# Kernel optimization log

Hardware: AMD Instinct MI355X
Metric: run time of the kernel (lower is better)

Reference implementation:

```python
import math
import jax, jax.numpy as jnp
import numpy as np

B, N, D, H, PREFIX = 2, 2048, 2048, 16, 512
HD = D // H
ROPE_BASE = 10000.0

def _rope(x):
    # x: [b, h, n, d]; rotate-half RoPE with positions 0..n-1
    d = x.shape[-1]
    n = x.shape[-2]
    inv_freq = 1.0 / (ROPE_BASE ** (jnp.arange(0, d, 2, dtype=jnp.float32) / d))  # [d/2]
    pos = jnp.arange(n, dtype=jnp.float32)
    freqs = pos[:, None] * inv_freq[None, :]            # [n, d/2]
    cos, sin = jnp.cos(freqs), jnp.sin(freqs)
    x1, x2 = x[..., : d // 2], x[..., d // 2 :]
    return jnp.concatenate([x1 * cos - x2 * sin, x2 * cos + x1 * sin], axis=-1).astype(x.dtype)

def setup_inputs() -> dict:
    key = jax.random.key(0)
    ks = jax.random.split(key, 6)
    x = jax.random.normal(ks[0], (B, N, D), dtype=jnp.float32)
    prefix_k = jax.random.normal(ks[1], (B, H, PREFIX, HD), dtype=jnp.float32)
    prefix_v = jax.random.normal(ks[2], (B, H, PREFIX, HD), dtype=jnp.float32)
    Wqkv = jax.random.normal(ks[3], (D, 3 * D), dtype=jnp.float32) * (D ** -0.5)
    bqkv = jnp.zeros((3 * D,), dtype=jnp.float32)
    Wff = jax.random.normal(ks[4], (D, D), dtype=jnp.float32) * (D ** -0.5)
    bff = jnp.zeros((D,), dtype=jnp.float32)
    # causal mask over current tokens; prefix (cache) columns fully visible
    causal = jnp.tril(jnp.ones((N, N), dtype=jnp.int32))
    mask = jnp.concatenate([jnp.ones((N, PREFIX), dtype=jnp.int32), causal], axis=1)[None, None]  # [1,1,N,N+PREFIX]
    return {"x": x, "mask": mask, "prefix_k": prefix_k, "prefix_v": prefix_v,
            "Wqkv": Wqkv, "bqkv": bqkv, "Wff": Wff, "bff": bff}

def reference(x, mask, prefix_k, prefix_v, Wqkv, bqkv, Wff, bff):
    b, n, d = x.shape
    h = prefix_k.shape[1]
    hd = d // h
    qkv = (x @ Wqkv + bqkv).reshape(b, n, 3, h, hd)      # 'b n (c h d)'
    qkv = jnp.transpose(qkv, (2, 0, 3, 1, 4))            # -> c b h n d
    q, k, v = qkv[0], qkv[1], qkv[2]
    k = jnp.concatenate([prefix_k, k], axis=2)           # [b,h,kt,hd]
    v = jnp.concatenate([prefix_v, v], axis=2)
    next_prefix_kv = jnp.stack([k, v])                   # cached BEFORE rope (as in source)
    q = _rope(q)
    k = _rope(k)
    scores = jnp.einsum('bhqd,bhkd->bhqk', q, k) / math.sqrt(hd)
    scores = jnp.where(mask == 0, jnp.finfo(scores.dtype).min, scores)
    probs = jax.nn.softmax(scores, axis=-1)              # dropout_prob=0.0 -> identity
    attn_o = jnp.einsum('bhqk,bhkd->bhqd', probs, v)
    attn_o = jnp.transpose(attn_o, (0, 2, 1, 3)).reshape(b, n, d)
    return attn_o @ Wff + bff, next_prefix_kv
```

## Files before the change

kernel.cpp:

```cpp
#include <hip/hip_runtime.h>
#include <hip/hip_bf16.h>
#include <stdint.h>

#define TPB 256

using f32x4 = __attribute__((ext_vector_type(4))) float;
using s16x8 = __attribute__((ext_vector_type(8))) short;
using s16x4 = __attribute__((ext_vector_type(4))) short;

__device__ __forceinline__ short f2bf(float f){
  union { float f; uint32_t u; } v; v.f = f;
  uint32_t u = v.u;
  uint32_t r = (u + 0x7fffu + ((u >> 16) & 1u)) >> 16;
  return (short)(uint16_t)r;
}
__device__ __forceinline__ float bf2f(short b){
  union { uint32_t u; float f; } v; v.u = ((uint32_t)(uint16_t)b) << 16;
  return v.f;
}
__device__ __forceinline__ f32x4 mfma16(s16x8 a, s16x8 b, f32x4 c){
  return __builtin_amdgcn_mfma_f32_16x16x32_bf16(a, b, c, 0, 0, 0);
}

#define AS1(p) ((const __attribute__((address_space(1))) void*)(p))
#define AS3(p) ((__attribute__((address_space(3))) void*)(p))

__global__ void k_cvt_bf16(const float* __restrict__ src, short* __restrict__ dst, int n8){
  int i = blockIdx.x * TPB + threadIdx.x;
  if (i >= n8) return;
  const float4* s4 = (const float4*)src;
  float4 a = s4[2*i], b = s4[2*i+1];
  s16x8 o;
  o[0]=f2bf(a.x); o[1]=f2bf(a.y); o[2]=f2bf(a.z); o[3]=f2bf(a.w);
  o[4]=f2bf(b.x); o[5]=f2bf(b.y); o[6]=f2bf(b.z); o[7]=f2bf(b.w);
  *(s16x8*)(dst + 8*(size_t)i) = o;
}

__global__ void k_trans_cvt(const float* __restrict__ W, short* __restrict__ WT, int K, int Nn){
  __shared__ float ls[32][33];
  int k0 = blockIdx.x * 32, n0 = blockIdx.y * 32;
  int c = threadIdx.x & 31, i = threadIdx.x >> 5;
#pragma unroll
  for (int rr = 0; rr < 4; rr++){
    int row = i*4 + rr;
    ls[row][c] = W[(size_t)(k0+row)*Nn + n0 + c];
  }
  __syncthreads();
#pragma unroll
  for (int rr = 0; rr < 4; rr++){
    int ro = i*4 + rr;
    WT[(size_t)(n0+ro)*K + k0 + c] = f2bf(ls[c][ro]);
  }
}

__global__ void __launch_bounds__(512, 2) k_gemm16(
    const short* __restrict__ A, const short* __restrict__ Bt,
    const float* __restrict__ bias,
    float* __restrict__ kvout,
    short* __restrict__ qpre, short* __restrict__ kpre, short* __restrict__ vpre)
{
  __shared__ __align__(16) short As[3][8192];
  __shared__ __align__(16) short Bs[3][8192];
  const int tid = threadIdx.x;
  const int w = tid >> 6, l = tid & 63;
  const int lrow = l & 15, lg = l >> 4;
  const int wm = w >> 2, wn = w & 3;
  const int lid = blockIdx.x + (int)gridDim.x * blockIdx.y;
  const int swz = (lid & 7) * 48 + (lid >> 3);
  const int m0 = (swz & 15) << 8, n0 = (swz >> 4) << 8;
  constexpr int NT = 64;

  f32x4 acc[8][4] = {};

  size_t offA0, offA1, offB0, offB1;
  {
    const int s0 = tid, s1 = 512 + tid;
    const int gr0 = ((s0 >> 6) << 4) + (s0 & 15), c80 = ((s0 >> 4) & 3) * 8;
    const int gr1 = ((s1 >> 6) << 4) + (s1 & 15), c81 = ((s1 >> 4) & 3) * 8;
    offA0 = (size_t)(m0 + gr0) * 2048 + c80;
    offA1 = (size_t)(m0 + gr1) * 2048 + c81;
    offB0 = (size_t)(n0 + gr0) * 2048 + c80;
    offB1 = (size_t)(n0 + gr1) * 2048 + c81;
  }
  const int dst0 = w * 1024;
  const int dst1 = 8192 + w * 1024;

#define STG_A0(sl, t_) __builtin_amdgcn_global_load_lds(AS1(A  + offA0 + (size_t)(t_)*32), AS3((char*)As[sl] + dst0), 16, 0, 0)
#define STG_A1(sl, t_) __builtin_amdgcn_global_load_lds(AS1(A  + offA1 + (size_t)(t_)*32), AS3((char*)As[sl] + dst1), 16, 0, 0)
#define STG_B0(sl, t_) __builtin_amdgcn_global_load_lds(AS1(Bt + offB0 + (size_t)(t_)*32), AS3((char*)Bs[sl] + dst0), 16, 0, 0)
#define STG_B1(sl, t_) __builtin_amdgcn_global_load_lds(AS1(Bt + offB1 + (size_t)(t_)*32), AS3((char*)Bs[sl] + dst1), 16, 0, 0)

  STG_A0(0,0); STG_A1(0,0); STG_B0(0,0); STG_B1(0,0);
  STG_A0(1,1); STG_A1(1,1); STG_B0(1,1); STG_B1(1,1);

  const int rdo  = lg * 256 + lrow * 16;
  const int aoff = wm * 8192 + rdo;
  const int boff = wn * 4096 + rdo;

  int slot = 0;
  for (int t = 0; t < NT; ++t){
    if (t < NT-1) asm volatile("s_waitcnt vmcnt(4)" ::: "memory");
    else          asm volatile("s_waitcnt vmcnt(0)" ::: "memory");
    __builtin_amdgcn_s_barrier();
    asm volatile("" ::: "memory");
    const int sslot = (slot == 0) ? 2 : slot - 1;
    const bool st = (t+2) < NT;
    const char* ab = (const char*)As[slot];
    const char* bb = (const char*)Bs[slot];

    s16x8 bfr[4];
#pragma unroll
    for (int ni = 0; ni < 4; ni++)
      bfr[ni] = *(const s16x8*)(bb + boff + ni*1024);
    s16x8 af[4];
#pragma unroll
    for (int mi = 0; mi < 4; mi++)
      af[mi] = *(const s16x8*)(ab + aoff + mi*1024);
    if (st){ STG_A0(sslot, t+2); STG_B0(sslot, t+2); }
    __builtin_amdgcn_s_setprio(1);
#pragma unroll
    for (int mi = 0; mi < 4; mi++)
#pragma unroll
      for (int ni = 0; ni < 4; ni++)
        acc[mi][ni] = mfma16(af[mi], bfr[ni], acc[mi][ni]);
    __builtin_amdgcn_s_setprio(0);
    asm volatile("" ::: "memory");
    __builtin_amdgcn_s_barrier();
    asm volatile("" ::: "memory");

    s16x8 af2[4];
#pragma unroll
    for (int mi = 0; mi < 4; mi++)
      af2[mi] = *(const s16x8*)(ab + aoff + (mi+4)*1024);
    if (st){ STG_A1(sslot, t+2); STG_B1(sslot, t+2); }
    __builtin_amdgcn_s_setprio(1);
#pragma unroll
    for (int mi = 0; mi < 4; mi++)
#pragma unroll
      for (int ni = 0; ni < 4; ni++)
        acc[mi+4][ni] = mfma16(af2[mi], bfr[ni], acc[mi+4][ni]);
    __builtin_amdgcn_s_setprio(0);
    slot = (slot == 2) ? 0 : slot + 1;
  }
#undef STG_A0
#undef STG_A1
#undef STG_B0
#undef STG_B1

#pragma unroll
  for (int mi = 0; mi < 8; mi++){
#pragma unroll
    for (int ni = 0; ni < 4; ni++){
      const int c  = n0 + wn*64 + ni*16 + lrow;
      const int mb = m0 + wm*128 + mi*16 + lg*4;
      const float bv = bias[c];
      const int s = c >> 11, h = (c >> 7) & 15, tt = c & 127;
#pragma unroll
      for (int r = 0; r < 4; r++){
        const int m = mb + r;
        const int b = m >> 11, n = m & 2047;
        const int bh = b*16 + h;
        const float val = acc[mi][ni][r] + bv;
        if (s == 0){
          qpre[((size_t)bh*2048 + n)*128 + tt] = f2bf(val);
        } else if (s == 1){
          kvout[((size_t)bh*2560 + 512 + n)*128 + tt] = val;
          kpre[((size_t)bh*2048 + n)*128 + tt] = f2bf(val);
        } else {
          kvout[(size_t)(32 + bh)*327680 + (size_t)(512 + n)*128 + tt] = val;
          vpre[((size_t)bh*2048 + n)*128 + tt] = f2bf(val);
        }
      }
    }
  }
}

template<int EPI>
__global__ void __launch_bounds__(512, 2) k_gemm8(
    const short* __restrict__ A, const short* __restrict__ Bt,
    int Nn, int K,
    const float* __restrict__ bias,
    float* __restrict__ outp,
    float* __restrict__ kvout,
    short* __restrict__ qpre, short* __restrict__ kpre, short* __restrict__ vpre)
{
  __shared__ __align__(16) short As[3][16384];
  __shared__ __align__(16) short Bs[3][8192];
  const int tid = threadIdx.x;
  const int w = tid >> 6, l = tid & 63;
  const int lrow = l & 15, lg = l >> 4;
  const int wm = w >> 1, wn = w & 1;
  const int m0 = blockIdx.x << 8, n0 = blockIdx.y << 7;
  const int NT = K >> 6;

  f32x4 acc[4][4] = {};

#define STAGE_A(slot, t, j) do {                                             \
    int chunk = ((w*4 + (j)) << 6) + l;                                      \
    int row = chunk >> 3, cc = chunk & 7;                                    \
    __builtin_amdgcn_global_load_lds(                                        \
      AS1(A + (size_t)(m0+row)*K + (t)*64 + ((cc ^ (row&7)) << 3)),          \
      AS3(&As[slot][(w*4 + (j)) << 9]), 16, 0, 0);                           \
  } while(0)
#define STAGE_B(slot, t, j) do {                                             \
    int chunk = ((w*2 + (j)) << 6) + l;                                      \
    int row = chunk >> 3, cc = chunk & 7;                                    \
    __builtin_amdgcn_global_load_lds(                                        \
      AS1(Bt + (size_t)(n0+row)*K + (t)*64 + ((cc ^ (row&7)) << 3)),         \
      AS3(&Bs[slot][(w*2 + (j)) << 9]), 16, 0, 0);                           \
  } while(0)

  STAGE_A(0,0,0); STAGE_A(0,0,1); STAGE_A(0,0,2); STAGE_A(0,0,3);
  STAGE_B(0,0,0); STAGE_B(0,0,1);
  STAGE_A(1,1,0); STAGE_A(1,1,1); STAGE_A(1,1,2); STAGE_A(1,1,3);
  STAGE_B(1,1,0); STAGE_B(1,1,1);

  int slot = 0;
  for (int t = 0; t < NT; ++t){
    if (t < NT-1) asm volatile("s_waitcnt vmcnt(6)" ::: "memory");
    else          asm volatile("s_waitcnt vmcnt(0)" ::: "memory");
    __builtin_amdgcn_s_barrier();
    asm volatile("" ::: "memory");
    const int sslot = (slot == 0) ? 2 : slot - 1;
    const bool st = (t+2) < NT;
    const char* ab = (const char*)As[slot];
    const char* bb = (const char*)Bs[slot];

    s16x8 bfr[4][2];
#pragma unroll
    for (int ni = 0; ni < 4; ni++){
      int row = wn*64 + ni*16 + lrow;
#pragma unroll
      for (int ks = 0; ks < 2; ks++)
        bfr[ni][ks] = *(const s16x8*)(bb + row*128 + ((ks*64 + lg*16) ^ ((row&7)<<4)));
    }
    s16x8 af[2][2];
#pragma unroll
    for (int mi = 0; mi < 2; mi++){
      int row = wm*64 + mi*16 + lrow;
#pragma unroll
      for (int ks = 0; ks < 2; ks++)
        af[mi][ks] = *(const s16x8*)(ab + row*128 + ((ks*64 + lg*16) ^ ((row&7)<<4)));
    }
    if (st){ STAGE_A(sslot,t+2,0); STAGE_A(sslot,t+2,1); STAGE_B(sslot,t+2,0); }
    __builtin_amdgcn_s_setprio(1);
#pragma unroll
    for (int ks = 0; ks < 2; ks++)
#pragma unroll
      for (int mi = 0; mi < 2; mi++)
#pragma unroll
        for (int ni = 0; ni < 4; ni++)
          acc[mi][ni] = mfma16(af[mi][ks], bfr[ni][ks], acc[mi][ni]);
    __builtin_amdgcn_s_setprio(0);
    asm volatile("" ::: "memory");
    __builtin_amdgcn_s_barrier();
    asm volatile("" ::: "memory");

    s16x8 af2[2][2];
#pragma unroll
    for (int mi = 0; mi < 2; mi++){
      int row = wm*64 + (mi+2)*16 + lrow;
#pragma unroll
      for (int ks = 0; ks < 2; ks++)
        af2[mi][ks] = *(const s16x8*)(ab + row*128 + ((ks*64 + lg*16) ^ ((row&7)<<4)));
    }
    if (st){ STAGE_A(sslot,t+2,2); STAGE_A(sslot,t+2,3); STAGE_B(sslot,t+2,1); }
    __builtin_amdgcn_s_setprio(1);
#pragma unroll
    for (int ks = 0; ks < 2; ks++)
#pragma unroll
      for (int mi = 0; mi < 2; mi++)
#pragma unroll
        for (int ni = 0; ni < 4; ni++)
          acc[mi+2][ni] = mfma16(af2[mi][ks], bfr[ni][ks], acc[mi+2][ni]);
    __builtin_amdgcn_s_setprio(0);
    slot = (slot == 2) ? 0 : slot + 1;
  }
#undef STAGE_A
#undef STAGE_B

#pragma unroll
  for (int mi = 0; mi < 4; mi++){
#pragma unroll
    for (int ni = 0; ni < 4; ni++){
      const int c  = n0 + wn*64 + ni*16 + lrow;
      const int mb = m0 + wm*64 + mi*16 + lg*4;
      const float bv = bias[c];
      if (EPI == 1){
#pragma unroll
        for (int r = 0; r < 4; r++)
          outp[(size_t)(mb+r)*Nn + c] = acc[mi][ni][r] + bv;
      } else {
        const int s = c >> 11, h = (c >> 7) & 15, tt = c & 127;
#pragma unroll
        for (int r = 0; r < 4; r++){
          const int m = mb + r;
          const int b = m >> 11, n = m & 2047;
          const int bh = b*16 + h;
          const float val = acc[mi][ni][r] + bv;
          if (s == 0){
            qpre[((size_t)bh*2048 + n)*128 + tt] = f2bf(val);
          } else if (s == 1){
            kvout[((size_t)bh*2560 + 512 + n)*128 + tt] = val;
            kpre[((size_t)bh*2048 + n)*128 + tt] = f2bf(val);
          } else {
            kvout[(size_t)(32 + bh)*327680 + (size_t)(512 + n)*128 + tt] = val;
            vpre[((size_t)bh*2048 + n)*128 + tt] = f2bf(val);
          }
        }
      }
    }
  }
}

__global__ void k_rope_q(const short* __restrict__ src, short* __restrict__ dst){
  int gid = blockIdx.x * TPB + threadIdx.x;
  int j = gid & 63; size_t row = gid >> 6;
  int n = (int)(row & 2047);
  float x1 = bf2f(src[row*128 + j]);
  float x2 = bf2f(src[row*128 + 64 + j]);
  float invf = __expf((float)j * (-9.210340371976184f/64.0f));
  float sn, cs; __sincosf((float)n * invf, &sn, &cs);
  const float sc = 0.088388347648318447f;
  dst[row*128 + j]      = f2bf((x1*cs - x2*sn) * sc);
  dst[row*128 + 64 + j] = f2bf((x2*cs + x1*sn) * sc);
}

__global__ void k_rope_k_new(const short* __restrict__ kpre, short* __restrict__ kr){
  int gid = blockIdx.x * TPB + threadIdx.x;
  int j = gid & 63; size_t row = gid >> 6;
  int bh = (int)(row >> 11), n = (int)(row & 2047);
  int pos = 512 + n;
  float x1 = bf2f(kpre[row*128 + j]);
  float x2 = bf2f(kpre[row*128 + 64 + j]);
  float invf = __expf((float)j * (-9.210340371976184f/64.0f));
  float sn, cs; __sincosf((float)pos * invf, &sn, &cs);
  size_t drow = (size_t)bh*2560 + pos;
  kr[drow*128 + j]      = f2bf(x1*cs - x2*sn);
  kr[drow*128 + 64 + j] = f2bf(x2*cs + x1*sn);
}

__global__ void k_rope_k_prefix(const float* __restrict__ pk, float* __restrict__ kvout0,
                                short* __restrict__ kr){
  int gid = blockIdx.x * TPB + threadIdx.x;
  int j = gid & 63; size_t row = gid >> 6;
  int bh = (int)(row >> 9), p = (int)(row & 511);
  float x1 = pk[row*128 + j];
  float x2 = pk[row*128 + 64 + j];
  size_t orow = (size_t)bh*2560 + p;
  kvout0[orow*128 + j]      = x1;
  kvout0[orow*128 + 64 + j] = x2;
  float invf = __expf((float)j * (-9.210340371976184f/64.0f));
  float sn, cs; __sincosf((float)p * invf, &sn, &cs);
  kr[orow*128 + j]      = f2bf(x1*cs - x2*sn);
  kr[orow*128 + 64 + j] = f2bf(x2*cs + x1*sn);
}

__global__ void k_v_prefix(const float* __restrict__ pv, float* __restrict__ kvout1,
                           short* __restrict__ vT){
  __shared__ float ls[32][129];
  int bh = blockIdx.x >> 4, pt = blockIdx.x & 15;
  int p0 = pt*32, tid = threadIdx.x;
#pragma unroll
  for (int i = 0; i < 16; i++){
    int idx = i*TPB + tid; int p = idx >> 7, t = idx & 127;
    float v = pv[((size_t)bh*512 + p0 + p)*128 + t];
    ls[p][t] = v;
    kvout1[((size_t)bh*2560 + p0 + p)*128 + t] = v;
  }
  __syncthreads();
#pragma unroll
  for (int i = 0; i < 16; i++){
    int idx = i*TPB + tid; int t = idx >> 5, p = idx & 31;
    vT[((size_t)bh*128 + t)*2560 + p0 + p] = f2bf(ls[p][t]);
  }
}

__global__ void k_v_new(const short* __restrict__ vpre, short* __restrict__ vT){
  __shared__ float ls[32][129];
  int bh = blockIdx.x >> 6, nt = blockIdx.x & 63;
  int n0 = nt*32, tid = threadIdx.x;
#pragma unroll
  for (int i = 0; i < 16; i++){
    int idx = i*TPB + tid; int p = idx >> 7, t = idx & 127;
    ls[p][t] = bf2f(vpre[((size_t)bh*2048 + n0 + p)*128 + t]);
  }
  __syncthreads();
#pragma unroll
  for (int i = 0; i < 16; i++){
    int idx = i*TPB + tid; int t = idx >> 5, p = idx & 31;
    vT[((size_t)bh*128 + t)*2560 + 512 + n0 + p] = f2bf(ls[p][t]);
  }
}

__global__ void __launch_bounds__(256, 2) k_attn(
    const short* __restrict__ qr, const short* __restrict__ kr,
    const short* __restrict__ vT, short* __restrict__ attno)
{
  __shared__ short Ks[2][64*128];
  __shared__ short VTs[2][128*64];
  __shared__ short Ps[4][16*64];
  const int bh = blockIdx.x;
  const int pA = blockIdx.y, pB = 31 - pA;
  const int nA = 9 + pA, nTot = 49;
  const int tid = threadIdx.x, w = tid >> 6, l = tid & 63;
  const int lrow = l & 15, lg = l >> 4;
  const int b = bh >> 4, h = bh & 15;

  s16x8 qfA[4], qfB[4];
  {
    const size_t rA = (size_t)bh*2048 + pA*64 + w*16 + lrow;
    const size_t rB = (size_t)bh*2048 + pB*64 + w*16 + lrow;
#pragma unroll
    for (int ks = 0; ks < 4; ks++){
      qfA[ks] = *(const s16x8*)&qr[rA*128 + ks*32 + lg*8];
      qfB[ks] = *(const s16x8*)&qr[rB*128 + ks*32 + lg*8];
    }
  }

#define STAGE_KV(buf, kv0s) do {                                                    \
    _Pragma("unroll")                                                               \
    for (int i_ = 0; i_ < 4; i_++){                                                 \
      int chunk = i_*256 + tid;                                                     \
      int row = chunk >> 4, cc = (chunk & 15) ^ (row & 7);                          \
      __builtin_amdgcn_global_load_lds(                                             \
        AS1(kr + ((size_t)bh*2560 + (kv0s) + row)*128 + cc*8),                      \
        AS3((char*)Ks[buf] + (i_*256 + w*64)*16), 16, 0, 0);                        \
    }                                                                               \
    _Pragma("unroll")                                                               \
    for (int i_ = 0; i_ < 4; i_++){                                                 \
      int chunk = i_*256 + tid;                                                     \
      int row = chunk >> 3, cc = (chunk & 7) ^ (row & 7);                           \
      __builtin_amdgcn_global_load_lds(                                             \
        AS1(vT + ((size_t)bh*128 + row)*2560 + (kv0s) + cc*8),                      \
        AS3((char*)VTs[buf] + (i_*256 + w*64)*16), 16, 0, 0);                       \
    }                                                                               \
  } while(0)

  STAGE_KV(0, 0);
  STAGE_KV(1, 64);

  char* psw = (char*)&Ps[w][0];
  int g = 0;
#pragma unroll 2
  for (int ph = 0; ph < 2; ph++){
    const int qt = ph ? pB : pA;
    const int n = 9 + qt;
    const int qbw = qt*64 + w*16;
    f32x4 acc[8] = {};
    float mr = -1e30f, lsum = 0.f;

    for (int t = 0; t < n; t++, g++){
      if (g+1 < nTot) asm volatile("s_waitcnt vmcnt(8)" ::: "memory");
      else            asm volatile("s_waitcnt vmcnt(0)" ::: "memory");
      __builtin_amdgcn_s_barrier();
      asm volatile("" ::: "memory");
      const char* kb_ = (const char*)Ks[g&1];
      const char* vb_ = (const char*)VTs[g&1];
      const int kv0 = t*64;

      f32x4 sf[4];
      __builtin_amdgcn_s_setprio(1);
#pragma unroll
      for (int kb = 0; kb < 4; kb++){
        f32x4 s = {0.f,0.f,0.f,0.f};
#pragma unroll
        for (int ks = 0; ks < 4; ks++){
          int row  = kb*16 + lrow;
          int colb = ks*64 + lg*16;
          s16x8 kf = *(const s16x8*)(kb_ + row*256 + (colb ^ ((row&7)<<4)));
          s = mfma16(kf, ph ? qfB[ks] : qfA[ks], s);
        }
        sf[kb] = s;
      }
      __builtin_amdgcn_s_setprio(0);

      const int qme = 512 + qbw + lrow;
      if (kv0 + 63 > 512 + qbw){
#pragma unroll
        for (int kb = 0; kb < 4; kb++)
#pragma unroll
          for (int r = 0; r < 4; r++){
            int kg = kv0 + kb*16 + lg*4 + r;
            if (kg > qme) sf[kb][r] = -1e30f;
          }
      }

      float m_ = fmaxf(
          fmaxf(fmaxf(fmaxf(sf[0][0],sf[0][1]),fmaxf(sf[0][2],sf[0][3])),
                fmaxf(fmaxf(sf[1][0],sf[1][1]),fmaxf(sf[1][2],sf[1][3]))),
          fmaxf(fmaxf(fmaxf(sf[2][0],sf[2][1]),fmaxf(sf[2][2],sf[2][3])),
                fmaxf(fmaxf(sf[3][0],sf[3][1]),fmaxf(sf[3][2],sf[3][3]))));
      m_ = fmaxf(m_, __shfl_xor(m_, 16));
      m_ = fmaxf(m_, __shfl_xor(m_, 32));

      if (__any(m_ > mr + 8.f)){
        float mnew = fmaxf(mr, m_);
        float sc = __expf(mr - mnew);
        mr = mnew;
        lsum *= sc;
        float scr[4];
#pragma unroll
        for (int r = 0; r < 4; r++)
          scr[r] = __shfl(sc, (l & 48) | (lg*4 + r));
#pragma unroll
        for (int dt = 0; dt < 8; dt++)
#pragma unroll
          for (int r = 0; r < 4; r++) acc[dt][r] *= scr[r];
      }

#pragma unroll
      for (int kb = 0; kb < 4; kb++){
        float p0 = __expf(sf[kb][0] - mr);
        float p1 = __expf(sf[kb][1] - mr);
        float p2 = __expf(sf[kb][2] - mr);
        float p3 = __expf(sf[kb][3] - mr);
        lsum += (p0+p1)+(p2+p3);
        s16x4 pk4 = { f2bf(p0), f2bf(p1), f2bf(p2), f2bf(p3) };
        *(s16x4*)(psw + (lrow*128 + ((kb*32 + lg*8) ^ ((lrow&7)<<4)))) = pk4;
      }

      __builtin_amdgcn_s_setprio(1);
#pragma unroll
      for (int kp = 0; kp < 2; kp++){
        s16x8 pa = *(const s16x8*)(psw + (lrow*128 + ((kp*64 + lg*16) ^ ((lrow&7)<<4))));
#pragma unroll
        for (int dt = 0; dt < 8; dt++){
          int vrow = dt*16 + lrow;
          int vcolb = kp*64 + lg*16;
          s16x8 vf = *(const s16x8*)(vb_ + vrow*128 + (vcolb ^ ((vrow&7)<<4)));
          acc[dt] = mfma16(pa, vf, acc[dt]);
        }
      }
      __builtin_amdgcn_s_setprio(0);

      asm volatile("" ::: "memory");
      __builtin_amdgcn_s_barrier();
      asm volatile("" ::: "memory");
      const int gg = g + 2;
      if (gg < nTot){
        const int kvs = (gg < nA ? gg : gg - nA) * 64;
        STAGE_KV(g&1, kvs);
      }
    }

    float ls_ = lsum;
    ls_ += __shfl_xor(ls_, 16);
    ls_ += __shfl_xor(ls_, 32);
    float linv[4];
#pragma unroll
    for (int r = 0; r < 4; r++)
      linv[r] = 1.f / __shfl(ls_, (l & 48) | (lg*4 + r));
#pragma unroll
    for (int dt = 0; dt < 8; dt++){
#pragma unroll
      for (int r = 0; r < 4; r++){
        int nrow = qbw + lg*4 + r;
        int dcol = h*128 + dt*16 + lrow;
        attno[((size_t)b*2048 + nrow)*2048 + dcol] = f2bf(acc[dt][r] * linv[r]);
      }
    }
  }
#undef STAGE_KV
}

extern "C" void kernel_launch(void* const* d_in, const int* in_sizes, int n_in,
                              void* d_out, int out_size, void* d_ws, size_t ws_size,
                              hipStream_t stream)
{
  const float* x    = (const float*)d_in[0];
  const float* pk   = (const float*)d_in[2];
  const float* pv   = (const float*)d_in[3];
  const float* Wqkv = (const float*)d_in[4];
  const float* bqkv = (const float*)d_in[5];
  const float* Wff  = (const float*)d_in[6];
  const float* bff  = (const float*)d_in[7];
  float* out   = (float*)d_out;
  float* kvout = out + 8388608;

  char* ws = (char*)d_ws;
  short* xb    = (short*)(ws);
  short* wqkvT = (short*)(ws + 16777216);
  short* wffT  = (short*)(ws + 41943040);
  short* qpre  = (short*)(ws + 50331648);
  short* kpre  = (short*)(ws + 67108864);
  short* vpre  = (short*)(ws + 83886080);
  short* qrp   = (short*)(ws + 100663296);
  short* krp   = (short*)(ws + 117440512);
  short* vTp   = (short*)(ws + 138412032);
  short* attno = (short*)(ws + 159383552);

  k_cvt_bf16<<<4096, TPB, 0, stream>>>(x, xb, 1048576);
  k_trans_cvt<<<dim3(64, 192), TPB, 0, stream>>>(Wqkv, wqkvT, 2048, 6144);
  k_trans_cvt<<<dim3(64, 64),  TPB, 0, stream>>>(Wff,  wffT,  2048, 2048);

  k_gemm16<<<dim3(16, 24), 512, 0, stream>>>(xb, wqkvT, bqkv, kvout, qpre, kpre, vpre);

  k_rope_q<<<16384, TPB, 0, stream>>>(qpre, qrp);
  k_rope_k_new<<<16384, TPB, 0, stream>>>(kpre, krp);
  k_rope_k_prefix<<<4096, TPB, 0, stream>>>(pk, kvout, krp);
  k_v_prefix<<<512, TPB, 0, stream>>>(pv, kvout + (size_t)32*327680, vTp);
  k_v_new<<<2048, TPB, 0, stream>>>(vpre, vTp);

  k_attn<<<dim3(32, 16), TPB, 0, stream>>>(qrp, krp, vTp, attno);

  k_gemm8<1><<<dim3(16, 16), 512, 0, stream>>>(attno, wffT, 2048, 2048, bff,
                                               out, nullptr, nullptr, nullptr, nullptr);
}
```

Measured before the change: 351.1 us.

## Restructure QKV GEMM mainloop to double-buffered K=64 tiles with quarter-step staging

Replaces the three-slot K=32 pipeline in the QKV projection GEMM with a two-buffer scheme that stages K=64 per iteration. Each iteration is split into four sub-phases that interleave LDS fragment reads, async global-to-LDS loads for the next tile, and MFMA blocks. This halves the outer loop count and aims to overlap prefetch more evenly with compute. In exchange it adds more barriers per iteration, and the prefetch distance drops to one tile.

```diff
diff --git a/kernel.cpp b/kernel.cpp
--- a/kernel.cpp
+++ b/kernel.cpp
@@ -59,8 +59,8 @@
     float* __restrict__ kvout,
     short* __restrict__ qpre, short* __restrict__ kpre, short* __restrict__ vpre)
 {
-  __shared__ __align__(16) short As[3][8192];
-  __shared__ __align__(16) short Bs[3][8192];
+  __shared__ __align__(16) short As[2][16384];
+  __shared__ __align__(16) short Bs[2][16384];
   const int tid = threadIdx.x;
   const int w = tid >> 6, l = tid & 63;
   const int lrow = l & 15, lg = l >> 4;
@@ -68,55 +68,49 @@
   const int lid = blockIdx.x + (int)gridDim.x * blockIdx.y;
   const int swz = (lid & 7) * 48 + (lid >> 3);
   const int m0 = (swz & 15) << 8, n0 = (swz >> 4) << 8;
-  constexpr int NT = 64;
+  constexpr int NT = 32;
 
   f32x4 acc[8][4] = {};
 
-  size_t offA0, offA1, offB0, offB1;
-  {
-    const int s0 = tid, s1 = 512 + tid;
-    const int gr0 = ((s0 >> 6) << 4) + (s0 & 15), c80 = ((s0 >> 4) & 3) * 8;
-    const int gr1 = ((s1 >> 6) << 4) + (s1 & 15), c81 = ((s1 >> 4) & 3) * 8;
-    offA0 = (size_t)(m0 + gr0) * 2048 + c80;
-    offA1 = (size_t)(m0 + gr1) * 2048 + c81;
-    offB0 = (size_t)(n0 + gr0) * 2048 + c80;
-    offB1 = (size_t)(n0 + gr1) * 2048 + c81;
-  }
-  const int dst0 = w * 1024;
-  const int dst1 = 8192 + w * 1024;
-
-#define STG_A0(sl, t_) __builtin_amdgcn_global_load_lds(AS1(A  + offA0 + (size_t)(t_)*32), AS3((char*)As[sl] + dst0), 16, 0, 0)
-#define STG_A1(sl, t_) __builtin_amdgcn_global_load_lds(AS1(A  + offA1 + (size_t)(t_)*32), AS3((char*)As[sl] + dst1), 16, 0, 0)
-#define STG_B0(sl, t_) __builtin_amdgcn_global_load_lds(AS1(Bt + offB0 + (size_t)(t_)*32), AS3((char*)Bs[sl] + dst0), 16, 0, 0)
-#define STG_B1(sl, t_) __builtin_amdgcn_global_load_lds(AS1(Bt + offB1 + (size_t)(t_)*32), AS3((char*)Bs[sl] + dst1), 16, 0, 0)
-
-  STG_A0(0,0); STG_A1(0,0); STG_B0(0,0); STG_B1(0,0);
-  STG_A0(1,1); STG_A1(1,1); STG_B0(1,1); STG_B1(1,1);
-
-  const int rdo  = lg * 256 + lrow * 16;
-  const int aoff = wm * 8192 + rdo;
-  const int boff = wn * 4096 + rdo;
-
-  int slot = 0;
+  const size_t gA0 = (size_t)(m0 + w*16 + (l & 15)) * 2048 + (l >> 4) * 8;
+  const size_t gB0 = (size_t)(n0 + w*16 + (l & 15)) * 2048 + (l >> 4) * 8;
+
+#define STG_A(buf, t_, j_, kk_)                                              \
+  __builtin_amdgcn_global_load_lds(                                          \
+    AS1(A + gA0 + (size_t)(j_)*262144 + (size_t)(t_)*64 + (kk_)*32),         \
+    AS3(&As[buf][((j_)*8 + w)*1024 + (kk_)*512]), 16, 0, 0)
+#define STG_B(buf, t_, j_, kk_)                                              \
+  __builtin_amdgcn_global_load_lds(                                          \
+    AS1(Bt + gB0 + (size_t)(j_)*262144 + (size_t)(t_)*64 + (kk_)*32),        \
+    AS3(&Bs[buf][((j_)*8 + w)*1024 + (kk_)*512]), 16, 0, 0)
+
+  STG_A(0, 0, 0, 0); STG_A(0, 0, 1, 0);
+  STG_B(0, 0, 0, 0); STG_B(0, 0, 1, 0);
+  STG_A(0, 0, 0, 1); STG_A(0, 0, 1, 1);
+  STG_B(0, 0, 0, 1); STG_B(0, 0, 1, 1);
+  asm volatile("s_waitcnt vmcnt(4)" ::: "memory");
+  __builtin_amdgcn_s_barrier();
+  asm volatile("" ::: "memory");
+
+  const int rdo = lg * 256 + lrow * 16;
+
+  int cb = 0;
   for (int t = 0; t < NT; ++t){
-    if (t < NT-1) asm volatile("s_waitcnt vmcnt(4)" ::: "memory");
-    else          asm volatile("s_waitcnt vmcnt(0)" ::: "memory");
-    __builtin_amdgcn_s_barrier();
-    asm volatile("" ::: "memory");
-    const int sslot = (slot == 0) ? 2 : slot - 1;
-    const bool st = (t+2) < NT;
-    const char* ab = (const char*)As[slot];
-    const char* bb = (const char*)Bs[slot];
-
-    s16x8 bfr[4];
+    const int nb = cb ^ 1;
+    const bool st = (t + 1) < NT;
+    const char* ab = (const char*)As[cb];
+    const char* bb = (const char*)Bs[cb];
+    s16x8 bfr[4], af[4];
+
 #pragma unroll
     for (int ni = 0; ni < 4; ni++)
-      bfr[ni] = *(const s16x8*)(bb + boff + ni*1024);
-    s16x8 af[4];
-#pragma unroll
-    for (int mi = 0; mi < 4; mi++)
-      af[mi] = *(const s16x8*)(ab + aoff + mi*1024);
-    if (st){ STG_A0(sslot, t+2); STG_B0(sslot, t+2); }
+      bfr[ni] = *(const s16x8*)(bb + (wn*4 + ni)*2048 + rdo);
+#pragma unroll
+    for (int mi = 0; mi < 4; mi++)
+      af[mi] = *(const s16x8*)(ab + (wm*8 + mi)*2048 + rdo);
+    if (st){ STG_A(nb, t+1, 0, 0); STG_A(nb, t+1, 1, 0); }
+    __builtin_amdgcn_s_barrier();
+    asm volatile("" ::: "memory");
     __builtin_amdgcn_s_setprio(1);
 #pragma unroll
     for (int mi = 0; mi < 4; mi++)
@@ -128,24 +122,67 @@
     __builtin_amdgcn_s_barrier();
     asm volatile("" ::: "memory");
 
-    s16x8 af2[4];
-#pragma unroll
-    for (int mi = 0; mi < 4; mi++)
-      af2[mi] = *(const s16x8*)(ab + aoff + (mi+4)*1024);
-    if (st){ STG_A1(sslot, t+2); STG_B1(sslot, t+2); }
+#pragma unroll
+    for (int mi = 0; mi < 4; mi++)
+      af[mi] = *(const s16x8*)(ab + (wm*8 + 4 + mi)*2048 + rdo);
+    if (st){ STG_B(nb, t+1, 0, 0); STG_B(nb, t+1, 1, 0); }
+    __builtin_amdgcn_s_barrier();
+    asm volatile("" ::: "memory");
     __builtin_amdgcn_s_setprio(1);
 #pragma unroll
     for (int mi = 0; mi < 4; mi++)
 #pragma unroll
       for (int ni = 0; ni < 4; ni++)
-        acc[mi+4][ni] = mfma16(af2[mi], bfr[ni], acc[mi+4][ni]);
+        acc[4+mi][ni] = mfma16(af[mi], bfr[ni], acc[4+mi][ni]);
     __builtin_amdgcn_s_setprio(0);
-    slot = (slot == 2) ? 0 : slot + 1;
-  }
-#undef STG_A0
-#undef STG_A1
-#undef STG_B0
-#undef STG_B1
+    if (t == NT-1) asm volatile("s_waitcnt vmcnt(0)" ::: "memory");
+    else           asm volatile("s_waitcnt vmcnt(4)" ::: "memory");
+    asm volatile("" ::: "memory");
+    __builtin_amdgcn_s_barrier();
+    asm volatile("" ::: "memory");
+
+#pragma unroll
+    for (int ni = 0; ni < 4; ni++)
+      bfr[ni] = *(const s16x8*)(bb + (wn*4 + ni)*2048 + 1024 + rdo);
+#pragma unroll
+    for (int mi = 0; mi < 4; mi++)
+      af[mi] = *(const s16x8*)(ab + (wm*8 + mi)*2048 + 1024 + rdo);
+    if (st){ STG_A(nb, t+1, 0, 1); STG_A(nb, t+1, 1, 1); }
+    __builtin_amdgcn_s_barrier();
+    asm volatile("" ::: "memory");
+    __builtin_amdgcn_s_setprio(1);
+#pragma unroll
+    for (int mi = 0; mi < 4; mi++)
+#pragma unroll
+      for (int ni = 0; ni < 4; ni++)
+        acc[mi][ni] = mfma16(af[mi], bfr[ni], acc[mi][ni]);
+    __builtin_amdgcn_s_setprio(0);
+    asm volatile("" ::: "memory");
+    __builtin_amdgcn_s_barrier();
+    asm volatile("" ::: "memory");
+
+#pragma unroll
+    for (int mi = 0; mi < 4; mi++)
+      af[mi] = *(const s16x8*)(ab + (wm*8 + 4 + mi)*2048 + 1024 + rdo);
+    if (st){ STG_B(nb, t+1, 0, 1); STG_B(nb, t+1, 1, 1); }
+    __builtin_amdgcn_s_barrier();
+    asm volatile("" ::: "memory");
+    __builtin_amdgcn_s_setprio(1);
+#pragma unroll
+    for (int mi = 0; mi < 4; mi++)
+#pragma unroll
+      for (int ni = 0; ni < 4; ni++)
+        acc[4+mi][ni] = mfma16(af[mi], bfr[ni], acc[4+mi][ni]);
+    __builtin_amdgcn_s_setprio(0);
+    asm volatile("s_waitcnt vmcnt(4)" ::: "memory");
+    asm volatile("" ::: "memory");
+    __builtin_amdgcn_s_barrier();
+    asm volatile("" ::: "memory");
+
+    cb = nb;
+  }
+#undef STG_A
+#undef STG_B
 
 #pragma unroll
   for (int mi = 0; mi < 8; mi++){
```

Result: slower. 404.8 us (+15.3%).
